# Performance work log

Measured on AMD Instinct MI355X. Metric: run time of the kernel, lower is better.

Reference implementation:

```python
import jax, jax.numpy as jnp
import numpy as np

N = 100000      # total nodes
E = 1600000     # total edges
B = 256         # graphs in batch
D_IN = 64       # node_in_dim
D_EMB = 128     # node_emb_dim
D_G = 128       # graph_emb_dim
L = 3           # gnn_layers
H1, H2 = 32, 8  # decoder MLP hidden dims
EPS_LN = 1e-5


def layernorm(h, g, b):
    mu = jnp.mean(h, -1, keepdims=True)
    var = jnp.mean((h - mu) ** 2, -1, keepdims=True)
    return (h - mu) * jax.lax.rsqrt(var + EPS_LN) * g + b


def setup_inputs() -> dict:
    key = jax.random.key(0)
    ks = jax.random.split(key, 16)
    gi = D_IN + D_EMB  # skip-conn GNN input dim

    def w(k, shape, fan):
        return jax.random.normal(k, shape, jnp.float32) / np.sqrt(fan).astype(np.float32)

    return {
        "x": jax.random.normal(ks[0], (N, D_IN), jnp.float32),
        "edge_index": jax.random.randint(ks[1], (2, E), 0, N),
        "batch_indices": jnp.sort(jax.random.randint(ks[2], (N,), 0, B)),
        "W_in": w(ks[3], (D_IN, D_EMB), D_IN), "b_in": jnp.zeros((D_EMB,), jnp.float32),
        "eps": jnp.zeros((L,), jnp.float32),  # GINConv train_eps init 0
        "mlp_W1": w(ks[4], (L, gi, D_EMB), gi), "mlp_b1": jnp.zeros((L, D_EMB), jnp.float32),
        "mlp_W2": w(ks[5], (L, D_EMB, D_EMB), D_EMB), "mlp_b2": jnp.zeros((L, D_EMB), jnp.float32),
        "ln_g": jnp.ones((L, D_EMB), jnp.float32), "ln_b": jnp.zeros((L, D_EMB), jnp.float32),
        "out_W": w(ks[6], (D_EMB, D_EMB), D_EMB), "out_b": jnp.zeros((D_EMB,), jnp.float32),
        "lnf_g": jnp.ones((D_EMB,), jnp.float32), "lnf_b": jnp.zeros((D_EMB,), jnp.float32),
        "graph_W": w(ks[7], (D_EMB, D_G), D_EMB), "graph_b": jnp.zeros((D_G,), jnp.float32),
        "gln_g": jnp.ones((D_G,), jnp.float32), "gln_b": jnp.zeros((D_G,), jnp.float32),
        "dW1": w(ks[8], (D_IN + D_EMB, H1), D_IN + D_EMB), "db1": jnp.zeros((H1,), jnp.float32),
        "dW2": w(ks[9], (H1, H2), H1), "db2": jnp.zeros((H2,), jnp.float32),
        "dW3": w(ks[10], (H2, 1), H2), "db3": jnp.zeros((1,), jnp.float32),
        "gW1": w(ks[11], (D_G, H1), D_G), "gb1": jnp.zeros((H1,), jnp.float32),
        "gW2": w(ks[12], (H1, H2), H1), "gb2": jnp.zeros((H2,), jnp.float32),
        "gW3": w(ks[13], (H2, 1), H2), "gb3": jnp.zeros((1,), jnp.float32),
    }


def reference(x, edge_index, batch_indices, W_in, b_in, eps, mlp_W1, mlp_b1, mlp_W2, mlp_b2,
              ln_g, ln_b, out_W, out_b, lnf_g, lnf_b, graph_W, graph_b, gln_g, gln_b,
              dW1, db1, dW2, db2, dW3, db3, gW1, gb1, gW2, gb2, gW3, gb3):
    src, dst = edge_index[0], edge_index[1]
    # Encoder: node_in_fc
    h = jax.nn.relu(x @ W_in + b_in)
    for l in range(L):
        gin = jnp.concatenate([x, h], -1)  # skip_conn: [N, D_IN+D_EMB]
        # GIN message passing: sum-aggregate neighbor features at target nodes
        agg = jax.ops.segment_sum(gin[src], dst, num_segments=N)
        z = (1.0 + eps[l]) * gin + agg
        z = jax.nn.relu(z @ mlp_W1[l] + mlp_b1[l]) @ mlp_W2[l] + mlp_b2[l]
        h = jax.nn.elu(layernorm(z, ln_g[l], ln_b[l]))
    # graph embedding: per-node fc+LN then global mean pool over batch segments
    ge = layernorm(jax.nn.relu(h @ graph_W + graph_b), gln_g, gln_b)
    sums = jax.ops.segment_sum(ge, batch_indices, num_segments=B)
    cnt = jax.ops.segment_sum(jnp.ones((N,), ge.dtype), batch_indices, num_segments=B)
    graph_emb = sums / jnp.maximum(cnt, 1.0)[:, None]
    # node_out_fc + final LN
    node_emb = layernorm(jax.nn.relu(h @ out_W + out_b), lnf_g, lnf_b)
    # Decoder: nodewise MLP on [x, node_emb] (skip_conn)
    ni = jnp.concatenate([x, node_emb], -1)
    no = jax.nn.relu(ni @ dW1 + db1)
    no = (jax.nn.relu(no @ dW2 + db2) @ dW3 + db3)[:, 0]  # [N]
    # graphwise residual MLP
    go = jax.nn.relu(graph_emb @ gW1 + gb1)
    go = (jax.nn.relu(go @ gW2 + gb2) @ gW3 + gb3)[:, 0]  # [B]
    return jnp.concatenate([no, go], -1)  # [N+B]
```

## Files before the change

kernel.cpp:

```cpp
#include <hip/hip_runtime.h>
#include <hip/hip_bf16.h>

#define D_IN 64
#define D_EMB 128
#define GI 192
#define H1 32
#define H2 8

typedef __attribute__((ext_vector_type(8))) short bf16x8;
typedef __attribute__((ext_vector_type(4))) float f32x4;

__device__ __forceinline__ unsigned short f2bf(float f) {
    unsigned int u = __float_as_uint(f);
    return (unsigned short)((u + 0x7fffu + ((u >> 16) & 1u)) >> 16);
}
__device__ __forceinline__ float bflo(unsigned int u) { return __uint_as_float(u << 16); }
__device__ __forceinline__ float bfhi(unsigned int u) { return __uint_as_float(u & 0xffff0000u); }
__device__ __forceinline__ unsigned int pk2(unsigned short a, unsigned short b) {
    return (unsigned int)a | ((unsigned int)b << 16);
}

__global__ __launch_bounds__(256) void hist_part_k(const int* __restrict__ dst, int* __restrict__ cnt,
                                                   int E, int N8) {
    int p = blockIdx.x & 7;
    int base = (blockIdx.x >> 3) * 1024;
    int lo = p * N8, hi = lo + N8;
    #pragma unroll
    for (int t = 0; t < 4; ++t) {
        int e = base + t * 256 + threadIdx.x;
        if (e < E) {
            int d = dst[e];
            if (d >= lo && d < hi) atomicAdd(&cnt[d], 1);
        }
    }
}

__global__ __launch_bounds__(256) void scan1_k(const int* __restrict__ cnt, int* __restrict__ loc,
                                               int* __restrict__ bsum, int N) {
    __shared__ int s[256];
    int tid = threadIdx.x;
    int i = blockIdx.x * 256 + tid;
    int v = (i < N) ? cnt[i] : 0;
    s[tid] = v;
    __syncthreads();
    #pragma unroll
    for (int off = 1; off < 256; off <<= 1) {
        int u = (tid >= off) ? s[tid - off] : 0;
        __syncthreads();
        s[tid] += u;
        __syncthreads();
    }
    int incl = s[tid];
    if (i < N) loc[i] = incl - v;
    if (tid == 255) bsum[blockIdx.x] = incl;
}

__global__ __launch_bounds__(512) void scan2_k(int* __restrict__ bsum, int NB) {
    __shared__ int s[512];
    int tid = threadIdx.x;
    int v = (tid < NB) ? bsum[tid] : 0;
    s[tid] = v;
    __syncthreads();
    #pragma unroll
    for (int off = 1; off < 512; off <<= 1) {
        int u = (tid >= off) ? s[tid - off] : 0;
        __syncthreads();
        s[tid] += u;
        __syncthreads();
    }
    if (tid < NB) bsum[tid] = s[tid] - v;
}

__global__ __launch_bounds__(256) void scan3_k(int* __restrict__ rp, const int* __restrict__ bsum,
                                               int* __restrict__ cursor, int N, int E) {
    int i = blockIdx.x * 256 + threadIdx.x;
    if (i < N) {
        int r = rp[i] + bsum[i >> 8];
        rp[i] = r;
        cursor[i] = r;
    } else if (i == N) {
        rp[N] = E;
    }
}

__global__ __launch_bounds__(256) void scatter_part_k(const int* __restrict__ src, const int* __restrict__ dst,
                                                      int* __restrict__ cursor, int* __restrict__ csr,
                                                      int E, int N8) {
    int p = blockIdx.x & 7;
    int base = (blockIdx.x >> 3) * 1024;
    int lo = p * N8, hi = lo + N8;
    #pragma unroll
    for (int t = 0; t < 4; ++t) {
        int e = base + t * 256 + threadIdx.x;
        if (e < E) {
            int d = dst[e];
            if (d >= lo && d < hi) {
                int s = src[e];
                int pos = atomicAdd(&cursor[d], 1);
                csr[pos] = s;
            }
        }
    }
}

__global__ __launch_bounds__(256) void xcvt_k(const float* __restrict__ x, unsigned short* __restrict__ xb,
                                              int total4) {
    int i = blockIdx.x * 256 + threadIdx.x;
    if (i < total4) {
        float4 v = ((const float4*)x)[i];
        ((uint2*)xb)[i] = make_uint2(pk2(f2bf(v.x), f2bf(v.y)), pk2(f2bf(v.z), f2bf(v.w)));
    }
}

__global__ __launch_bounds__(256) void wfrag_all_k(
    const float* __restrict__ W_in, const float* __restrict__ mlp_W1, const float* __restrict__ mlp_W2,
    const float* __restrict__ graph_W, const float* __restrict__ out_W,
    unsigned short* __restrict__ wf_in, unsigned short* __restrict__ wf_w1,
    unsigned short* __restrict__ wf_w2, unsigned short* __restrict__ wf_graph,
    unsigned short* __restrict__ wf_out) {
    int idx = blockIdx.x * 256 + threadIdx.x;
    const float* src;
    unsigned short* dst;
    int local;
    if (idx < 8192) { src = W_in; dst = wf_in; local = idx; }
    else if (idx < 81920) { int t = idx - 8192; int l = t / 24576; local = t - l * 24576;
                            src = mlp_W1 + (size_t)l * 24576; dst = wf_w1 + (size_t)l * 24576; }
    else if (idx < 131072) { int t = idx - 81920; int l = t / 16384; local = t - l * 16384;
                             src = mlp_W2 + (size_t)l * 16384; dst = wf_w2 + (size_t)l * 16384; }
    else if (idx < 147456) { local = idx - 131072; src = graph_W; dst = wf_graph; }
    else { local = idx - 147456; src = out_W; dst = wf_out; }
    int k = local >> 7, c = local & 127;
    dst[(((size_t)(k >> 3) * 128) + c) * 8 + (k & 7)] = f2bf(src[local]);
}

__global__ __launch_bounds__(256) void agg64b_k(const unsigned short* __restrict__ xb,
                                                const int* __restrict__ rp, const int* __restrict__ cs,
                                                unsigned short* __restrict__ outb, int N) {
    int n = blockIdx.x * 8 + (threadIdx.x >> 5);
    int lane = threadIdx.x & 31;
    if (n >= N) return;
    int bg = rp[n], e = rp[n + 1];
    const unsigned int* x2 = (const unsigned int*)xb;
    float sx = 0.f, sy = 0.f;
    int j = bg;
    for (; j + 3 < e; j += 4) {
        unsigned int v0 = x2[(size_t)cs[j] * 32 + lane];
        unsigned int v1 = x2[(size_t)cs[j + 1] * 32 + lane];
        unsigned int v2 = x2[(size_t)cs[j + 2] * 32 + lane];
        unsigned int v3 = x2[(size_t)cs[j + 3] * 32 + lane];
        sx += bflo(v0) + bflo(v1) + bflo(v2) + bflo(v3);
        sy += bfhi(v0) + bfhi(v1) + bfhi(v2) + bfhi(v3);
    }
    for (; j < e; ++j) {
        unsigned int v = x2[(size_t)cs[j] * 32 + lane];
        sx += bflo(v);
        sy += bfhi(v);
    }
    ((unsigned int*)outb)[(size_t)n * 32 + lane] = pk2(f2bf(sx), f2bf(sy));
}

__global__ __launch_bounds__(256) void aggz_k(const unsigned short* __restrict__ hb,
                                              const int* __restrict__ rp, const int* __restrict__ cs,
                                              const float* __restrict__ epsp,
                                              unsigned short* __restrict__ zh, int N) {
    int w = threadIdx.x >> 6, lane = threadIdx.x & 63;
    int n = blockIdx.x * 4 + w;
    if (n >= N) return;
    float es = 1.0f + epsp[0];
    int bg = rp[n], e = rp[n + 1];
    const unsigned int* h2 = (const unsigned int*)hb;
    float sx = 0.f, sy = 0.f;
    int j = bg;
    for (; j + 3 < e; j += 4) {
        unsigned int v0 = h2[(size_t)cs[j] * 64 + lane];
        unsigned int v1 = h2[(size_t)cs[j + 1] * 64 + lane];
        unsigned int v2 = h2[(size_t)cs[j + 2] * 64 + lane];
        unsigned int v3 = h2[(size_t)cs[j + 3] * 64 + lane];
        sx += bflo(v0) + bflo(v1) + bflo(v2) + bflo(v3);
        sy += bfhi(v0) + bfhi(v1) + bfhi(v2) + bfhi(v3);
    }
    for (; j < e; ++j) {
        unsigned int v = h2[(size_t)cs[j] * 64 + lane];
        sx += bflo(v);
        sy += bfhi(v);
    }
    unsigned int hv = h2[(size_t)n * 64 + lane];
    sx = fmaf(es, bflo(hv), sx);
    sy = fmaf(es, bfhi(hv), sy);
    ((unsigned int*)zh)[(size_t)n * 64 + lane] = pk2(f2bf(sx), f2bf(sy));
}

template <int RELU, int ELU>
__device__ __forceinline__ void ln_epilogue(
    f32x4 (&acc)[4][4], const float* __restrict__ bias,
    const float* __restrict__ g, const float* __restrict__ b,
    unsigned short* __restrict__ out,
    int rowBase, int wr, int wc, int lg, int l15, int wh,
    float* rsum, float* rsq, int N) {
    float bv[4], gv[4], bbv[4];
    #pragma unroll
    for (int cb = 0; cb < 4; ++cb) {
        int col = wc + cb * 16 + l15;
        bv[cb] = bias[col];
        gv[cb] = g[col];
        bbv[cb] = b[col];
    }
    float ps[4][4], pq[4][4];
    #pragma unroll
    for (int rb = 0; rb < 4; ++rb)
        #pragma unroll
        for (int q = 0; q < 4; ++q) {
            float s = 0.f, sq = 0.f;
            #pragma unroll
            for (int cb = 0; cb < 4; ++cb) {
                float v = acc[rb][cb][q] + bv[cb];
                if (RELU) v = fmaxf(v, 0.f);
                s += v;
                sq += v * v;
            }
            ps[rb][q] = s;
            pq[rb][q] = sq;
        }
    #pragma unroll
    for (int m = 1; m < 16; m <<= 1) {
        #pragma unroll
        for (int rb = 0; rb < 4; ++rb)
            #pragma unroll
            for (int q = 0; q < 4; ++q) {
                ps[rb][q] += __shfl_xor(ps[rb][q], m, 64);
                pq[rb][q] += __shfl_xor(pq[rb][q], m, 64);
            }
    }
    if (l15 == 0) {
        #pragma unroll
        for (int rb = 0; rb < 4; ++rb)
            #pragma unroll
            for (int q = 0; q < 4; ++q) {
                int row = wr + rb * 16 + lg * 4 + q;
                rsum[wh * 128 + row] = ps[rb][q];
                rsq[wh * 128 + row] = pq[rb][q];
            }
    }
    __syncthreads();
    #pragma unroll
    for (int rb = 0; rb < 4; ++rb)
        #pragma unroll
        for (int q = 0; q < 4; ++q) {
            int row = wr + rb * 16 + lg * 4 + q;
            float st = rsum[row] + rsum[128 + row];
            float sqt = rsq[row] + rsq[128 + row];
            float mu = st * (1.f / 128.f);
            float var = sqt * (1.f / 128.f) - mu * mu;
            float rs = rsqrtf(var + 1e-5f);
            int grow = rowBase + row;
            if (grow < N) {
                #pragma unroll
                for (int cb = 0; cb < 4; ++cb) {
                    float v = acc[rb][cb][q] + bv[cb];
                    if (RELU) v = fmaxf(v, 0.f);
                    float y = (v - mu) * rs * gv[cb] + bbv[cb];
                    if (ELU) y = y > 0.f ? y : expm1f(y);
                    out[(size_t)grow * D_EMB + wc + cb * 16 + l15] = f2bf(y);
                }
            }
        }
}

__global__ __launch_bounds__(256) void enc_gemm_k(
    const unsigned short* __restrict__ Abf, const unsigned short* __restrict__ Wf,
    const float* __restrict__ bias, unsigned short* __restrict__ C, int N) {
    __shared__ unsigned short As[4 * 128 * 8];
    const int tid = threadIdx.x;
    const int wid = tid >> 6, lane = tid & 63;
    const int l15 = lane & 15, lg = lane >> 4;
    const int rowBase = blockIdx.x * 128;
    const int wr = (wid >> 1) * 64, wc = (wid & 1) * 64;
    f32x4 zero = {0.f, 0.f, 0.f, 0.f};
    f32x4 acc[4][4];
    #pragma unroll
    for (int i = 0; i < 4; ++i)
        #pragma unroll
        for (int j = 0; j < 4; ++j) acc[i][j] = zero;
    const int r = tid >> 1, hp = tid & 1;
    const int arow = min(rowBase + r, N - 1);

    for (int k0 = 0; k0 < D_IN; k0 += 32) {
        bf16x8 bfr[4];
        const int G = (k0 >> 3) + lg;
        #pragma unroll
        for (int cb = 0; cb < 4; ++cb)
            bfr[cb] = *(const bf16x8*)&Wf[(((size_t)G * 128) + wc + cb * 16 + l15) * 8];
        __syncthreads();
        #pragma unroll
        for (int g2 = 0; g2 < 2; ++g2) {
            int gg = hp * 2 + g2;
            int k = k0 + gg * 8;
            uint4 w = *(const uint4*)(Abf + (size_t)arow * D_IN + k);
            *(uint4*)&As[(((size_t)gg * 128) + r) * 8] = w;
        }
        __syncthreads();
        #pragma unroll
        for (int rb = 0; rb < 4; ++rb) {
            bf16x8 afr = *(const bf16x8*)&As[(((size_t)lg * 128) + wr + rb * 16 + l15) * 8];
            #pragma unroll
            for (int cb = 0; cb < 4; ++cb)
                acc[rb][cb] = __builtin_amdgcn_mfma_f32_16x16x32_bf16(afr, bfr[cb], acc[rb][cb], 0, 0, 0);
        }
    }
    #pragma unroll
    for (int cb = 0; cb < 4; ++cb) {
        int col = wc + cb * 16 + l15;
        float bvv = bias[col];
        #pragma unroll
        for (int rb = 0; rb < 4; ++rb)
            #pragma unroll
            for (int q = 0; q < 4; ++q) {
                int row = rowBase + wr + rb * 16 + lg * 4 + q;
                if (row < N) C[(size_t)row * D_EMB + col] = f2bf(fmaxf(acc[rb][cb][q] + bvv, 0.f));
            }
    }
}

__global__ __launch_bounds__(256) void gin_layer_k(
    const unsigned short* __restrict__ xb, const unsigned short* __restrict__ aggxb,
    const unsigned short* __restrict__ zhb, const float* __restrict__ epsp,
    const unsigned short* __restrict__ W1f, const float* __restrict__ b1,
    const unsigned short* __restrict__ W2f, const float* __restrict__ b2,
    const float* __restrict__ lng, const float* __restrict__ lnb,
    unsigned short* __restrict__ hbo, int N) {
    __shared__ unsigned short As[4 * 128 * 8];
    __shared__ unsigned short T1[16 * 128 * 8];
    __shared__ float rsum[2 * 128];
    __shared__ float rsq[2 * 128];

    const int tid = threadIdx.x;
    const int wid = tid >> 6, lane = tid & 63;
    const int l15 = lane & 15, lg = lane >> 4;
    const int rowBase = blockIdx.x * 128;
    const int wr = (wid >> 1) * 64, wc = (wid & 1) * 64;
    const int wh = wid & 1;

    f32x4 zero = {0.f, 0.f, 0.f, 0.f};
    f32x4 acc[4][4];
    #pragma unroll
    for (int i = 0; i < 4; ++i)
        #pragma unroll
        for (int j = 0; j < 4; ++j) acc[i][j] = zero;

    const float es = 1.0f + epsp[0];
    const int r = tid >> 1, hp = tid & 1;
    const int arow = min(rowBase + r, N - 1);

    for (int k0 = 0; k0 < GI; k0 += 32) {
        bf16x8 bfr[4];
        const int G = (k0 >> 3) + lg;
        #pragma unroll
        for (int cb = 0; cb < 4; ++cb)
            bfr[cb] = *(const bf16x8*)&W1f[(((size_t)G * 128) + wc + cb * 16 + l15) * 8];
        __syncthreads();
        #pragma unroll
        for (int g2 = 0; g2 < 2; ++g2) {
            int gg = hp * 2 + g2;
            int k = k0 + gg * 8;
            uint4 w;
            if (k < D_IN) {
                uint4 xv = *(const uint4*)(xb + (size_t)arow * D_IN + k);
                uint4 av = *(const uint4*)(aggxb + (size_t)arow * D_IN + k);
                unsigned short o[8];
                o[0] = f2bf(fmaf(es, bflo(xv.x), bflo(av.x)));
                o[1] = f2bf(fmaf(es, bfhi(xv.x), bfhi(av.x)));
                o[2] = f2bf(fmaf(es, bflo(xv.y), bflo(av.y)));
                o[3] = f2bf(fmaf(es, bfhi(xv.y), bfhi(av.y)));
                o[4] = f2bf(fmaf(es, bflo(xv.z), bflo(av.z)));
                o[5] = f2bf(fmaf(es, bfhi(xv.z), bfhi(av.z)));
                o[6] = f2bf(fmaf(es, bflo(xv.w), bflo(av.w)));
                o[7] = f2bf(fmaf(es, bfhi(xv.w), bfhi(av.w)));
                w = make_uint4(pk2(o[0], o[1]), pk2(o[2], o[3]), pk2(o[4], o[5]), pk2(o[6], o[7]));
            } else {
                w = *(const uint4*)(zhb + (size_t)arow * D_EMB + (k - D_IN));
            }
            *(uint4*)&As[(((size_t)gg * 128) + r) * 8] = w;
        }
        __syncthreads();
        #pragma unroll
        for (int rb = 0; rb < 4; ++rb) {
            bf16x8 afr = *(const bf16x8*)&As[(((size_t)lg * 128) + wr + rb * 16 + l15) * 8];
            #pragma unroll
            for (int cb = 0; cb < 4; ++cb)
                acc[rb][cb] = __builtin_amdgcn_mfma_f32_16x16x32_bf16(afr, bfr[cb], acc[rb][cb], 0, 0, 0);
        }
    }

    #pragma unroll
    for (int cb = 0; cb < 4; ++cb) {
        int col = wc + cb * 16 + l15;
        float bvv = b1[col];
        #pragma unroll
        for (int rb = 0; rb < 4; ++rb)
            #pragma unroll
            for (int q = 0; q < 4; ++q) {
                int row = wr + rb * 16 + lg * 4 + q;
                float v = fmaxf(acc[rb][cb][q] + bvv, 0.f);
                T1[(((size_t)(col >> 3) * 128) + row) * 8 + (col & 7)] = f2bf(v);
            }
    }
    __syncthreads();

    f32x4 acc2[4][4];
    #pragma unroll
    for (int i = 0; i < 4; ++i)
        #pragma unroll
        for (int j = 0; j < 4; ++j) acc2[i][j] = zero;
    for (int k0 = 0; k0 < D_EMB; k0 += 32) {
        bf16x8 bfr[4];
        const int G = (k0 >> 3) + lg;
        #pragma unroll
        for (int cb = 0; cb < 4; ++cb)
            bfr[cb] = *(const bf16x8*)&W2f[(((size_t)G * 128) + wc + cb * 16 + l15) * 8];
        #pragma unroll
        for (int rb = 0; rb < 4; ++rb) {
            bf16x8 afr = *(const bf16x8*)&T1[(((size_t)G * 128) + wr + rb * 16 + l15) * 8];
            #pragma unroll
            for (int cb = 0; cb < 4; ++cb)
                acc2[rb][cb] = __builtin_amdgcn_mfma_f32_16x16x32_bf16(afr, bfr[cb], acc2[rb][cb], 0, 0, 0);
        }
    }

    ln_epilogue<0, 1>(acc2, b2, lng, lnb, hbo, rowBase, wr, wc, lg, l15, wh, rsum, rsq, N);
}

__global__ __launch_bounds__(256) void fc2_k(
    const unsigned short* __restrict__ Abf,
    const unsigned short* __restrict__ WfG, const float* __restrict__ biasG,
    const float* __restrict__ gG, const float* __restrict__ bG, unsigned short* __restrict__ outG,
    const unsigned short* __restrict__ WfN, const float* __restrict__ biasN,
    const float* __restrict__ gN, const float* __restrict__ bN, unsigned short* __restrict__ outN,
    int N) {
    __shared__ unsigned short As[4 * 128 * 8];
    __shared__ float rsum[2 * 128];
    __shared__ float rsq[2 * 128];
    const int tid = threadIdx.x;
    const int wid = tid >> 6, lane = tid & 63;
    const int l15 = lane & 15, lg = lane >> 4;
    const int rowBase = blockIdx.x * 128;
    const int wr = (wid >> 1) * 64, wc = (wid & 1) * 64;
    const int wh = wid & 1;
    f32x4 zero = {0.f, 0.f, 0.f, 0.f};
    f32x4 accG[4][4], accN[4][4];
    #pragma unroll
    for (int i = 0; i < 4; ++i)
        #pragma unroll
        for (int j = 0; j < 4; ++j) { accG[i][j] = zero; accN[i][j] = zero; }
    const int r = tid >> 1, hp = tid & 1;
    const int arow = min(rowBase + r, N - 1);

    for (int k0 = 0; k0 < D_EMB; k0 += 32) {
        bf16x8 bfrG[4], bfrN[4];
        const int G = (k0 >> 3) + lg;
        #pragma unroll
        for (int cb = 0; cb < 4; ++cb) {
            bfrG[cb] = *(const bf16x8*)&WfG[(((size_t)G * 128) + wc + cb * 16 + l15) * 8];
            bfrN[cb] = *(const bf16x8*)&WfN[(((size_t)G * 128) + wc + cb * 16 + l15) * 8];
        }
        __syncthreads();
        #pragma unroll
        for (int g2 = 0; g2 < 2; ++g2) {
            int gg = hp * 2 + g2;
            int k = k0 + gg * 8;
            uint4 w = *(const uint4*)(Abf + (size_t)arow * D_EMB + k);
            *(uint4*)&As[(((size_t)gg * 128) + r) * 8] = w;
        }
        __syncthreads();
        #pragma unroll
        for (int rb = 0; rb < 4; ++rb) {
            bf16x8 afr = *(const bf16x8*)&As[(((size_t)lg * 128) + wr + rb * 16 + l15) * 8];
            #pragma unroll
            for (int cb = 0; cb < 4; ++cb) {
                accG[rb][cb] = __builtin_amdgcn_mfma_f32_16x16x32_bf16(afr, bfrG[cb], accG[rb][cb], 0, 0, 0);
                accN[rb][cb] = __builtin_amdgcn_mfma_f32_16x16x32_bf16(afr, bfrN[cb], accN[rb][cb], 0, 0, 0);
            }
        }
    }
    ln_epilogue<1, 0>(accG, biasG, gG, bG, outG, rowBase, wr, wc, lg, l15, wh, rsum, rsq, N);
    __syncthreads();
    ln_epilogue<1, 0>(accN, biasN, gN, bN, outN, rowBase, wr, wc, lg, l15, wh, rsum, rsq, N);
}

__global__ __launch_bounds__(256) void bounds_k(const int* __restrict__ batch, int* __restrict__ bounds,
                                                int N, int B) {
    int i = blockIdx.x * 256 + threadIdx.x;
    if (i <= B) {
        int lo = 0, hi = N;
        while (lo < hi) { int m = (lo + hi) >> 1; if (batch[m] < i) lo = m + 1; else hi = m; }
        bounds[i] = lo;
    }
}

__global__ __launch_bounds__(128) void pool_part_k(const unsigned short* __restrict__ ge,
                                                   const int* __restrict__ bounds,
                                                   float* __restrict__ gemb) {
    int b = blockIdx.x >> 3;
    int s = blockIdx.x & 7;
    int start = bounds[b], end = bounds[b + 1];
    int len = end - start;
    int c0 = start + (int)(((long long)len * s) >> 3);
    int c1 = start + (int)(((long long)len * (s + 1)) >> 3);
    if (c1 <= c0) return;
    int col = threadIdx.x;
    float sum = 0.f;
    for (int n = c0; n < c1; ++n)
        sum += __uint_as_float((unsigned int)ge[(size_t)n * D_EMB + col] << 16);
    atomicAdd(&gemb[(size_t)b * D_EMB + col], sum);
}

__global__ __launch_bounds__(256) void node_dec_k(
    const float* __restrict__ x, const unsigned short* __restrict__ ne,
    const float* __restrict__ W1, const float* __restrict__ b1,
    const float* __restrict__ W2, const float* __restrict__ b2,
    const float* __restrict__ W3, const float* __restrict__ b3,
    float* __restrict__ out, int N) {
    __shared__ float W1s[GI * H1];
    __shared__ float W2s[H1 * H2];
    __shared__ float W3s[H2];
    __shared__ float b1s[H1], b2s[H2];
    for (int i = threadIdx.x; i < GI * H1; i += 256) W1s[i] = W1[i];
    if (threadIdx.x < H1 * H2) W2s[threadIdx.x] = W2[threadIdx.x];
    if (threadIdx.x < H2) { W3s[threadIdx.x] = W3[threadIdx.x]; b2s[threadIdx.x] = b2[threadIdx.x]; }
    if (threadIdx.x < H1) b1s[threadIdx.x] = b1[threadIdx.x];
    __syncthreads();
    int n = blockIdx.x * 256 + threadIdx.x;
    if (n >= N) return;
    float acc[H1];
    #pragma unroll
    for (int j = 0; j < H1; ++j) acc[j] = b1s[j];
    const float4* xr = (const float4*)(x + (size_t)n * D_IN);
    #pragma unroll 4
    for (int q = 0; q < D_IN / 4; ++q) {
        float4 v = xr[q];
        int k = q * 4;
        #pragma unroll
        for (int j = 0; j < H1; ++j) acc[j] = fmaf(v.x, W1s[(k + 0) * H1 + j], acc[j]);
        #pragma unroll
        for (int j = 0; j < H1; ++j) acc[j] = fmaf(v.y, W1s[(k + 1) * H1 + j], acc[j]);
        #pragma unroll
        for (int j = 0; j < H1; ++j) acc[j] = fmaf(v.z, W1s[(k + 2) * H1 + j], acc[j]);
        #pragma unroll
        for (int j = 0; j < H1; ++j) acc[j] = fmaf(v.w, W1s[(k + 3) * H1 + j], acc[j]);
    }
    const uint4* nr = (const uint4*)(ne + (size_t)n * D_EMB);
    #pragma unroll 4
    for (int q = 0; q < 16; ++q) {
        uint4 v = nr[q];
        float f[8] = {bflo(v.x), bfhi(v.x), bflo(v.y), bfhi(v.y),
                      bflo(v.z), bfhi(v.z), bflo(v.w), bfhi(v.w)};
        int k = D_IN + q * 8;
        #pragma unroll
        for (int e = 0; e < 8; ++e) {
            #pragma unroll
            for (int j = 0; j < H1; ++j) acc[j] = fmaf(f[e], W1s[(k + e) * H1 + j], acc[j]);
        }
    }
    #pragma unroll
    for (int j = 0; j < H1; ++j) acc[j] = fmaxf(acc[j], 0.f);
    float a2[H2];
    #pragma unroll
    for (int m = 0; m < H2; ++m) a2[m] = b2s[m];
    #pragma unroll
    for (int j = 0; j < H1; ++j)
        #pragma unroll
        for (int m = 0; m < H2; ++m) a2[m] = fmaf(acc[j], W2s[j * H2 + m], a2[m]);
    float o = b3[0];
    #pragma unroll
    for (int m = 0; m < H2; ++m) o = fmaf(fmaxf(a2[m], 0.f), W3s[m], o);
    out[n] = o;
}

__global__ __launch_bounds__(256) void graph_dec_k(
    const float* __restrict__ gemb, const int* __restrict__ bounds,
    const float* __restrict__ W1, const float* __restrict__ b1,
    const float* __restrict__ W2, const float* __restrict__ b2,
    const float* __restrict__ W3, const float* __restrict__ b3,
    float* __restrict__ out, int B) {
    __shared__ float W1s[D_EMB * H1];
    __shared__ float W2s[H1 * H2];
    __shared__ float W3s[H2];
    __shared__ float b1s[H1], b2s[H2];
    for (int i = threadIdx.x; i < D_EMB * H1; i += 256) W1s[i] = W1[i];
    if (threadIdx.x < H1 * H2) W2s[threadIdx.x] = W2[threadIdx.x];
    if (threadIdx.x < H2) { W3s[threadIdx.x] = W3[threadIdx.x]; b2s[threadIdx.x] = b2[threadIdx.x]; }
    if (threadIdx.x < H1) b1s[threadIdx.x] = b1[threadIdx.x];
    __syncthreads();
    int gidx = threadIdx.x;
    if (gidx >= B) return;
    int len = bounds[gidx + 1] - bounds[gidx];
    float inv = 1.f / fmaxf((float)len, 1.f);
    float acc[H1];
    #pragma unroll
    for (int j = 0; j < H1; ++j) acc[j] = b1s[j];
    const float4* gr = (const float4*)(gemb + (size_t)gidx * D_EMB);
    for (int q = 0; q < D_EMB / 4; ++q) {
        float4 v = gr[q];
        v.x *= inv; v.y *= inv; v.z *= inv; v.w *= inv;
        int k = q * 4;
        #pragma unroll
        for (int j = 0; j < H1; ++j) acc[j] = fmaf(v.x, W1s[(k + 0) * H1 + j], acc[j]);
        #pragma unroll
        for (int j = 0; j < H1; ++j) acc[j] = fmaf(v.y, W1s[(k + 1) * H1 + j], acc[j]);
        #pragma unroll
        for (int j = 0; j < H1; ++j) acc[j] = fmaf(v.z, W1s[(k + 2) * H1 + j], acc[j]);
        #pragma unroll
        for (int j = 0; j < H1; ++j) acc[j] = fmaf(v.w, W1s[(k + 3) * H1 + j], acc[j]);
    }
    #pragma unroll
    for (int j = 0; j < H1; ++j) acc[j] = fmaxf(acc[j], 0.f);
    float a2[H2];
    #pragma unroll
    for (int m = 0; m < H2; ++m) a2[m] = b2s[m];
    #pragma unroll
    for (int j = 0; j < H1; ++j)
        #pragma unroll
        for (int m = 0; m < H2; ++m) a2[m] = fmaf(acc[j], W2s[j * H2 + m], a2[m]);
    float o = b3[0];
    #pragma unroll
    for (int m = 0; m < H2; ++m) o = fmaf(fmaxf(a2[m], 0.f), W3s[m], o);
    out[gidx] = o;
}

extern "C" void kernel_launch(void* const* d_in, const int* in_sizes, int n_in,
                              void* d_out, int out_size, void* d_ws, size_t ws_size,
                              hipStream_t stream) {
    const float* x       = (const float*)d_in[0];
    const int*   ei      = (const int*)d_in[1];
    const int*   batch   = (const int*)d_in[2];
    const float* W_in    = (const float*)d_in[3];
    const float* b_in    = (const float*)d_in[4];
    const float* eps     = (const float*)d_in[5];
    const float* mlp_W1  = (const float*)d_in[6];
    const float* mlp_b1  = (const float*)d_in[7];
    const float* mlp_W2  = (const float*)d_in[8];
    const float* mlp_b2  = (const float*)d_in[9];
    const float* ln_g    = (const float*)d_in[10];
    const float* ln_b    = (const float*)d_in[11];
    const float* out_W   = (const float*)d_in[12];
    const float* out_b   = (const float*)d_in[13];
    const float* lnf_g   = (const float*)d_in[14];
    const float* lnf_b   = (const float*)d_in[15];
    const float* graph_W = (const float*)d_in[16];
    const float* graph_b = (const float*)d_in[17];
    const float* gln_g   = (const float*)d_in[18];
    const float* gln_b   = (const float*)d_in[19];
    const float* dW1     = (const float*)d_in[20];
    const float* db1     = (const float*)d_in[21];
    const float* dW2     = (const float*)d_in[22];
    const float* db2     = (const float*)d_in[23];
    const float* dW3     = (const float*)d_in[24];
    const float* db3     = (const float*)d_in[25];
    const float* gW1     = (const float*)d_in[26];
    const float* gb1     = (const float*)d_in[27];
    const float* gW2     = (const float*)d_in[28];
    const float* gb2     = (const float*)d_in[29];
    const float* gW3     = (const float*)d_in[30];
    const float* gb3     = (const float*)d_in[31];
    float* out = (float*)d_out;

    const int N = in_sizes[0] / D_IN;
    const int E = in_sizes[1] / 2;
    const int B = out_size - N;
    const int N8 = (N + 7) / 8;

    const int* esrc = ei;
    const int* edst = ei + E;

    size_t off = 0;
    auto alloc = [&](size_t bytes) { size_t o = off; off += (bytes + 255) & ~(size_t)255; return o; };
    char* ws = (char*)d_ws;
    unsigned short* xb    = (unsigned short*)(ws + alloc((size_t)N * D_IN * 2));
    unsigned short* hb0   = (unsigned short*)(ws + alloc((size_t)N * D_EMB * 2));
    unsigned short* hb1   = (unsigned short*)(ws + alloc((size_t)N * D_EMB * 2));
    unsigned short* zh    = (unsigned short*)(ws + alloc((size_t)N * D_EMB * 2));
    unsigned short* aggxb = (unsigned short*)(ws + alloc((size_t)N * D_IN * 2));
    float* gemb = (float*)(ws + alloc((size_t)B * D_EMB * 4));
    unsigned short* wfpool = (unsigned short*)(ws + alloc((size_t)163840 * 2));
    int* row_ptr = (int*)(ws + alloc((size_t)(N + 1) * 4));
    int* cnt     = (int*)(ws + alloc((size_t)N * 4));
    int* bsum    = (int*)(ws + alloc(512 * 4));
    int* bounds  = (int*)(ws + alloc((size_t)(B + 1) * 4));
    int* csr     = (int*)(ws + alloc((size_t)E * 4));
    (void)ws_size;

    unsigned short* wf_in    = wfpool;
    unsigned short* wf_w1    = wf_in + (size_t)64 * 128;
    unsigned short* wf_w2    = wf_w1 + (size_t)3 * 192 * 128;
    unsigned short* wf_graph = wf_w2 + (size_t)3 * 128 * 128;
    unsigned short* wf_out   = wf_graph + (size_t)128 * 128;

    const int NB = (N + 255) / 256;
    const int gridEP = 8 * ((E + 1023) / 1024);
    const int gridN4 = (N + 3) / 4;
    const int gridG = (N + 127) / 128;

    hipMemsetAsync(cnt, 0, (size_t)N * 4, stream);
    hist_part_k<<<gridEP, 256, 0, stream>>>(edst, cnt, E, N8);
    scan1_k<<<NB, 256, 0, stream>>>(cnt, row_ptr, bsum, N);
    scan2_k<<<1, 512, 0, stream>>>(bsum, NB);
    scan3_k<<<(N + 256) / 256, 256, 0, stream>>>(row_ptr, bsum, cnt, N, E);
    scatter_part_k<<<gridEP, 256, 0, stream>>>(esrc, edst, cnt, csr, E, N8);

    xcvt_k<<<(N * D_IN / 4 + 255) / 256, 256, 0, stream>>>(x, xb, N * D_IN / 4);
    wfrag_all_k<<<640, 256, 0, stream>>>(W_in, mlp_W1, mlp_W2, graph_W, out_W,
                                         wf_in, wf_w1, wf_w2, wf_graph, wf_out);
    bounds_k<<<(B + 256) / 256, 256, 0, stream>>>(batch, bounds, N, B);
    hipMemsetAsync(gemb, 0, (size_t)B * D_EMB * 4, stream);

    agg64b_k<<<(N + 7) / 8, 256, 0, stream>>>(xb, row_ptr, csr, aggxb, N);

    enc_gemm_k<<<gridG, 256, 0, stream>>>(xb, wf_in, b_in, hb0, N);

    unsigned short* hin = hb0;
    unsigned short* hout = hb1;
    for (int l = 0; l < 3; ++l) {
        aggz_k<<<gridN4, 256, 0, stream>>>(hin, row_ptr, csr, eps + l, zh, N);
        gin_layer_k<<<gridG, 256, 0, stream>>>(xb, aggxb, zh, eps + l,
                                               wf_w1 + (size_t)l * 192 * 128, mlp_b1 + (size_t)l * D_EMB,
                                               wf_w2 + (size_t)l * 128 * 128, mlp_b2 + (size_t)l * D_EMB,
                                               ln_g + (size_t)l * D_EMB, ln_b + (size_t)l * D_EMB,
                                               hout, N);
        unsigned short* t = hin; hin = hout; hout = t;
    }
    unsigned short* zb  = hb0;
    unsigned short* neb = zh;

    fc2_k<<<gridG, 256, 0, stream>>>(hin,
                                     wf_graph, graph_b, gln_g, gln_b, zb,
                                     wf_out, out_b, lnf_g, lnf_b, neb, N);
    pool_part_k<<<B * 8, 128, 0, stream>>>(zb, bounds, gemb);

    node_dec_k<<<(N + 255) / 256, 256, 0, stream>>>(x, neb, dW1, db1, dW2, db2, dW3, db3, out, N);
    graph_dec_k<<<1, 256, 0, stream>>>(gemb, bounds, gW1, gb1, gW2, gb2, gW3, gb3, out + N, B);
}
```

Baseline: 819.9 us.

## Load MFMA A-fragments directly from global and precompute per-layer x-part inputs

GEMM kernels now read A operand fragments straight from global memory into registers instead of staging through LDS with two barriers per k-step. A new kernel precomputes (1+eps_l)*x + agg(x) for all three layers once, so gin_layer_k no longer recomputes it per layer. The T1 intermediate buffer is halved by processing the hidden layer in two 64-column chunks, which raises occupancy but adds a barrier. The trade-off is extra global traffic for three N×64 buffers and less coalesced fragment loads.

```diff
diff --git a/kernel.cpp b/kernel.cpp
--- a/kernel.cpp
+++ b/kernel.cpp
@@ -159,6 +159,23 @@
     ((unsigned int*)outb)[(size_t)n * 32 + lane] = pk2(f2bf(sx), f2bf(sy));
 }
 
+__global__ __launch_bounds__(256) void zxcvt_k(const unsigned short* __restrict__ xb,
+                                               const unsigned short* __restrict__ aggxb,
+                                               const float* __restrict__ eps,
+                                               unsigned short* __restrict__ zx0,
+                                               unsigned short* __restrict__ zx1,
+                                               unsigned short* __restrict__ zx2, int total2) {
+    int i = blockIdx.x * 256 + threadIdx.x;
+    if (i >= total2) return;
+    unsigned int xv = ((const unsigned int*)xb)[i];
+    unsigned int av = ((const unsigned int*)aggxb)[i];
+    float xl = bflo(xv), xh = bfhi(xv), al = bflo(av), ah = bfhi(av);
+    float e0 = 1.0f + eps[0], e1 = 1.0f + eps[1], e2 = 1.0f + eps[2];
+    ((unsigned int*)zx0)[i] = pk2(f2bf(fmaf(e0, xl, al)), f2bf(fmaf(e0, xh, ah)));
+    ((unsigned int*)zx1)[i] = pk2(f2bf(fmaf(e1, xl, al)), f2bf(fmaf(e1, xh, ah)));
+    ((unsigned int*)zx2)[i] = pk2(f2bf(fmaf(e2, xl, al)), f2bf(fmaf(e2, xh, ah)));
+}
+
 __global__ __launch_bounds__(256) void aggz_k(const unsigned short* __restrict__ hb,
                                               const int* __restrict__ rp, const int* __restrict__ cs,
                                               const float* __restrict__ epsp,
@@ -269,7 +286,6 @@
 __global__ __launch_bounds__(256) void enc_gemm_k(
     const unsigned short* __restrict__ Abf, const unsigned short* __restrict__ Wf,
     const float* __restrict__ bias, unsigned short* __restrict__ C, int N) {
-    __shared__ unsigned short As[4 * 128 * 8];
     const int tid = threadIdx.x;
     const int wid = tid >> 6, lane = tid & 63;
     const int l15 = lane & 15, lg = lane >> 4;
@@ -281,27 +297,20 @@
     for (int i = 0; i < 4; ++i)
         #pragma unroll
         for (int j = 0; j < 4; ++j) acc[i][j] = zero;
-    const int r = tid >> 1, hp = tid & 1;
-    const int arow = min(rowBase + r, N - 1);
+    const unsigned short* ap[4];
+    #pragma unroll
+    for (int rb = 0; rb < 4; ++rb)
+        ap[rb] = Abf + (size_t)min(rowBase + wr + rb * 16 + l15, N - 1) * D_IN;
 
     for (int k0 = 0; k0 < D_IN; k0 += 32) {
+        const int G = (k0 >> 3) + lg;
         bf16x8 bfr[4];
-        const int G = (k0 >> 3) + lg;
         #pragma unroll
         for (int cb = 0; cb < 4; ++cb)
             bfr[cb] = *(const bf16x8*)&Wf[(((size_t)G * 128) + wc + cb * 16 + l15) * 8];
-        __syncthreads();
-        #pragma unroll
-        for (int g2 = 0; g2 < 2; ++g2) {
-            int gg = hp * 2 + g2;
-            int k = k0 + gg * 8;
-            uint4 w = *(const uint4*)(Abf + (size_t)arow * D_IN + k);
-            *(uint4*)&As[(((size_t)gg * 128) + r) * 8] = w;
-        }
-        __syncthreads();
         #pragma unroll
         for (int rb = 0; rb < 4; ++rb) {
-            bf16x8 afr = *(const bf16x8*)&As[(((size_t)lg * 128) + wr + rb * 16 + l15) * 8];
+            bf16x8 afr = *(const bf16x8*)(ap[rb] + G * 8);
             #pragma unroll
             for (int cb = 0; cb < 4; ++cb)
                 acc[rb][cb] = __builtin_amdgcn_mfma_f32_16x16x32_bf16(afr, bfr[cb], acc[rb][cb], 0, 0, 0);
@@ -322,14 +331,12 @@
 }
 
 __global__ __launch_bounds__(256) void gin_layer_k(
-    const unsigned short* __restrict__ xb, const unsigned short* __restrict__ aggxb,
-    const unsigned short* __restrict__ zhb, const float* __restrict__ epsp,
+    const unsigned short* __restrict__ zxl, const unsigned short* __restrict__ zhb,
     const unsigned short* __restrict__ W1f, const float* __restrict__ b1,
     const unsigned short* __restrict__ W2f, const float* __restrict__ b2,
     const float* __restrict__ lng, const float* __restrict__ lnb,
     unsigned short* __restrict__ hbo, int N) {
-    __shared__ unsigned short As[4 * 128 * 8];
-    __shared__ unsigned short T1[16 * 128 * 8];
+    __shared__ unsigned short T1[8 * 128 * 8];
     __shared__ float rsum[2 * 128];
     __shared__ float rsq[2 * 128];
 
@@ -347,82 +354,85 @@
         #pragma unroll
         for (int j = 0; j < 4; ++j) acc[i][j] = zero;
 
-    const float es = 1.0f + epsp[0];
-    const int r = tid >> 1, hp = tid & 1;
-    const int arow = min(rowBase + r, N - 1);
-
-    for (int k0 = 0; k0 < GI; k0 += 32) {
+    const unsigned short* axp[4];
+    const unsigned short* ahp[4];
+    #pragma unroll
+    for (int rb = 0; rb < 4; ++rb) {
+        int ar = min(rowBase + wr + rb * 16 + l15, N - 1);
+        axp[rb] = zxl + (size_t)ar * D_IN;
+        ahp[rb] = zhb + (size_t)ar * D_EMB;
+    }
+
+    for (int k0 = 0; k0 < D_IN; k0 += 32) {
+        const int G = (k0 >> 3) + lg;
         bf16x8 bfr[4];
-        const int G = (k0 >> 3) + lg;
         #pragma unroll
         for (int cb = 0; cb < 4; ++cb)
             bfr[cb] = *(const bf16x8*)&W1f[(((size_t)G * 128) + wc + cb * 16 + l15) * 8];
-        __syncthreads();
-        #pragma unroll
-        for (int g2 = 0; g2 < 2; ++g2) {
-            int gg = hp * 2 + g2;
-            int k = k0 + gg * 8;
-            uint4 w;
-            if (k < D_IN) {
-                uint4 xv = *(const uint4*)(xb + (size_t)arow * D_IN + k);
-                uint4 av = *(const uint4*)(aggxb + (size_t)arow * D_IN + k);
-                unsigned short o[8];
-                o[0] = f2bf(fmaf(es, bflo(xv.x), bflo(av.x)));
-                o[1] = f2bf(fmaf(es, bfhi(xv.x), bfhi(av.x)));
-                o[2] = f2bf(fmaf(es, bflo(xv.y), bflo(av.y)));
-                o[3] = f2bf(fmaf(es, bfhi(xv.y), bfhi(av.y)));
-                o[4] = f2bf(fmaf(es, bflo(xv.z), bflo(av.z)));
-                o[5] = f2bf(fmaf(es, bfhi(xv.z), bfhi(av.z)));
-                o[6] = f2bf(fmaf(es, bflo(xv.w), bflo(av.w)));
-                o[7] = f2bf(fmaf(es, bfhi(xv.w), bfhi(av.w)));
-                w = make_uint4(pk2(o[0], o[1]), pk2(o[2], o[3]), pk2(o[4], o[5]), pk2(o[6], o[7]));
-            } else {
-                w = *(const uint4*)(zhb + (size_t)arow * D_EMB + (k - D_IN));
-            }
-            *(uint4*)&As[(((size_t)gg * 128) + r) * 8] = w;
-        }
-        __syncthreads();
         #pragma unroll
         for (int rb = 0; rb < 4; ++rb) {
-            bf16x8 afr = *(const bf16x8*)&As[(((size_t)lg * 128) + wr + rb * 16 + l15) * 8];
+            bf16x8 afr = *(const bf16x8*)(axp[rb] + G * 8);
             #pragma unroll
             for (int cb = 0; cb < 4; ++cb)
                 acc[rb][cb] = __builtin_amdgcn_mfma_f32_16x16x32_bf16(afr, bfr[cb], acc[rb][cb], 0, 0, 0);
         }
     }
-
-    #pragma unroll
-    for (int cb = 0; cb < 4; ++cb) {
-        int col = wc + cb * 16 + l15;
-        float bvv = b1[col];
-        #pragma unroll
-        for (int rb = 0; rb < 4; ++rb)
-            #pragma unroll
-            for (int q = 0; q < 4; ++q) {
-                int row = wr + rb * 16 + lg * 4 + q;
-                float v = fmaxf(acc[rb][cb][q] + bvv, 0.f);
-                T1[(((size_t)(col >> 3) * 128) + row) * 8 + (col & 7)] = f2bf(v);
-            }
-    }
-    __syncthreads();
+    for (int k0 = D_IN; k0 < GI; k0 += 32) {
+        const int G = (k0 >> 3) + lg;
+        const int ZG = ((k0 - D_IN) >> 3) + lg;
+        bf16x8 bfr[4];
+        #pragma unroll
+        for (int cb = 0; cb < 4; ++cb)
+            bfr[cb] = *(const bf16x8*)&W1f[(((size_t)G * 128) + wc + cb * 16 + l15) * 8];
+        #pragma unroll
+        for (int rb = 0; rb < 4; ++rb) {
+            bf16x8 afr = *(const bf16x8*)(ahp[rb] + ZG * 8);
+            #pragma unroll
+            for (int cb = 0; cb < 4; ++cb)
+                acc[rb][cb] = __builtin_amdgcn_mfma_f32_16x16x32_bf16(afr, bfr[cb], acc[rb][cb], 0, 0, 0);
+        }
+    }
 
     f32x4 acc2[4][4];
     #pragma unroll
     for (int i = 0; i < 4; ++i)
         #pragma unroll
         for (int j = 0; j < 4; ++j) acc2[i][j] = zero;
-    for (int k0 = 0; k0 < D_EMB; k0 += 32) {
-        bf16x8 bfr[4];
-        const int G = (k0 >> 3) + lg;
-        #pragma unroll
-        for (int cb = 0; cb < 4; ++cb)
-            bfr[cb] = *(const bf16x8*)&W2f[(((size_t)G * 128) + wc + cb * 16 + l15) * 8];
-        #pragma unroll
-        for (int rb = 0; rb < 4; ++rb) {
-            bf16x8 afr = *(const bf16x8*)&T1[(((size_t)G * 128) + wr + rb * 16 + l15) * 8];
+
+    #pragma unroll
+    for (int c = 0; c < 2; ++c) {
+        if (c) __syncthreads();
+        if (wc == c * 64) {
+            #pragma unroll
+            for (int cb = 0; cb < 4; ++cb) {
+                int col = wc + cb * 16 + l15;
+                int tcol = col - c * 64;
+                float bvv = b1[col];
+                #pragma unroll
+                for (int rb = 0; rb < 4; ++rb)
+                    #pragma unroll
+                    for (int q = 0; q < 4; ++q) {
+                        int row = wr + rb * 16 + lg * 4 + q;
+                        float v = fmaxf(acc[rb][cb][q] + bvv, 0.f);
+                        T1[(((size_t)(tcol >> 3) * 128) + row) * 8 + (tcol & 7)] = f2bf(v);
+                    }
+            }
+        }
+        __syncthreads();
+        for (int k0 = c * 64; k0 < c * 64 + 64; k0 += 32) {
+            const int G = (k0 >> 3) + lg;
+            const int TG = G - c * 8;
+            bf16x8 bfr[4];
             #pragma unroll
             for (int cb = 0; cb < 4; ++cb)
-                acc2[rb][cb] = __builtin_amdgcn_mfma_f32_16x16x32_bf16(afr, bfr[cb], acc2[rb][cb], 0, 0, 0);
+                bfr[cb] = *(const bf16x8*)&W2f[(((size_t)G * 128) + wc + cb * 16 + l15) * 8];
+            #pragma unroll
+            for (int rb = 0; rb < 4; ++rb) {
+                bf16x8 afr = *(const bf16x8*)&T1[(((size_t)TG * 128) + wr + rb * 16 + l15) * 8];
+                #pragma unroll
+                for (int cb = 0; cb < 4; ++cb)
+                    acc2[rb][cb] = __builtin_amdgcn_mfma_f32_16x16x32_bf16(afr, bfr[cb], acc2[rb][cb], 0, 0, 0);
+            }
         }
     }
 
@@ -436,7 +446,6 @@
     const unsigned short* __restrict__ WfN, const float* __restrict__ biasN,
     const float* __restrict__ gN, const float* __restrict__ bN, unsigned short* __restrict__ outN,
     int N) {
-    __shared__ unsigned short As[4 * 128 * 8];
     __shared__ float rsum[2 * 128];
     __shared__ float rsq[2 * 128];
     const int tid = threadIdx.x;
@@ -451,29 +460,22 @@
     for (int i = 0; i < 4; ++i)
         #pragma unroll
         for (int j = 0; j < 4; ++j) { accG[i][j] = zero; accN[i][j] = zero; }
-    const int r = tid >> 1, hp = tid & 1;
-    const int arow = min(rowBase + r, N - 1);
+    const unsigned short* ap[4];
+    #pragma unroll
+    for (int rb = 0; rb < 4; ++rb)
+        ap[rb] = Abf + (size_t)min(rowBase + wr + rb * 16 + l15, N - 1) * D_EMB;
 
     for (int k0 = 0; k0 < D_EMB; k0 += 32) {
+        const int G = (k0 >> 3) + lg;
         bf16x8 bfrG[4], bfrN[4];
-        const int G = (k0 >> 3) + lg;
         #pragma unroll
         for (int cb = 0; cb < 4; ++cb) {
             bfrG[cb] = *(const bf16x8*)&WfG[(((size_t)G * 128) + wc + cb * 16 + l15) * 8];
             bfrN[cb] = *(const bf16x8*)&WfN[(((size_t)G * 128) + wc + cb * 16 + l15) * 8];
         }
-        __syncthreads();
-        #pragma unroll
-        for (int g2 = 0; g2 < 2; ++g2) {
-            int gg = hp * 2 + g2;
-            int k = k0 + gg * 8;
-            uint4 w = *(const uint4*)(Abf + (size_t)arow * D_EMB + k);
-            *(uint4*)&As[(((size_t)gg * 128) + r) * 8] = w;
-        }
-        __syncthreads();
         #pragma unroll
         for (int rb = 0; rb < 4; ++rb) {
-            bf16x8 afr = *(const bf16x8*)&As[(((size_t)lg * 128) + wr + rb * 16 + l15) * 8];
+            bf16x8 afr = *(const bf16x8*)(ap[rb] + G * 8);
             #pragma unroll
             for (int cb = 0; cb < 4; ++cb) {
                 accG[rb][cb] = __builtin_amdgcn_mfma_f32_16x16x32_bf16(afr, bfrG[cb], accG[rb][cb], 0, 0, 0);
@@ -679,6 +681,9 @@
     unsigned short* hb1   = (unsigned short*)(ws + alloc((size_t)N * D_EMB * 2));
     unsigned short* zh    = (unsigned short*)(ws + alloc((size_t)N * D_EMB * 2));
     unsigned short* aggxb = (unsigned short*)(ws + alloc((size_t)N * D_IN * 2));
+    unsigned short* zx0   = (unsigned short*)(ws + alloc((size_t)N * D_IN * 2));
+    unsigned short* zx1   = (unsigned short*)(ws + alloc((size_t)N * D_IN * 2));
+    unsigned short* zx2   = (unsigned short*)(ws + alloc((size_t)N * D_IN * 2));
     float* gemb = (float*)(ws + alloc((size_t)B * D_EMB * 4));
     unsigned short* wfpool = (unsigned short*)(ws + alloc((size_t)163840 * 2));
     int* row_ptr = (int*)(ws + alloc((size_t)(N + 1) * 4));
@@ -694,6 +699,8 @@
     unsigned short* wf_graph = wf_w2 + (size_t)3 * 128 * 128;
     unsigned short* wf_out   = wf_graph + (size_t)128 * 128;
 
+    unsigned short* zxs[3] = {zx0, zx1, zx2};
+
     const int NB = (N + 255) / 256;
     const int gridEP = 8 * ((E + 1023) / 1024);
     const int gridN4 = (N + 3) / 4;
@@ -713,6 +720,7 @@
     hipMemsetAsync(gemb, 0, (size_t)B * D_EMB * 4, stream);
 
     agg64b_k<<<(N + 7) / 8, 256, 0, stream>>>(xb, row_ptr, csr, aggxb, N);
+    zxcvt_k<<<(N * 32 + 255) / 256, 256, 0, stream>>>(xb, aggxb, eps, zx0, zx1, zx2, N * 32);
 
     enc_gemm_k<<<gridG, 256, 0, stream>>>(xb, wf_in, b_in, hb0, N);
 
@@ -720,7 +728,7 @@
     unsigned short* hout = hb1;
     for (int l = 0; l < 3; ++l) {
         aggz_k<<<gridN4, 256, 0, stream>>>(hin, row_ptr, csr, eps + l, zh, N);
-        gin_layer_k<<<gridG, 256, 0, stream>>>(xb, aggxb, zh, eps + l,
+        gin_layer_k<<<gridG, 256, 0, stream>>>(zxs[l], zh,
                                                wf_w1 + (size_t)l * 192 * 128, mlp_b1 + (size_t)l * D_EMB,
                                                wf_w2 + (size_t)l * 128 * 128, mlp_b2 + (size_t)l * D_EMB,
                                                ln_g + (size_t)l * D_EMB, ln_b + (size_t)l * D_EMB,
```

New measurement: 931.4 us. 1.14x slower.
